# Optimization experiments

Measured on AMD Instinct MI355X. Metric: run time of the kernel, lower is better.

## Reference

```python
import jax, jax.numpy as jnp
import numpy as np

N = 50000       # original graph nodes (= number of subgraphs, one per node)
S = 10          # nodes per subgraph
M = N * S       # combined subgraph nodes
E = 2_000_000   # combined subgraph edges
E0 = 1_000_000  # original edges
NIN, HOP, NOUT, L = 64, 16, 128, 3
D = NIN + HOP   # conv width (80)


def setup_inputs() -> dict:
    key = jax.random.key(0)
    ks = iter(jax.random.split(key, 40))
    rng = np.random.default_rng(0)

    # structured index tensors: subgraph b occupies rows [b*S, (b+1)*S); row b*S is the centroid
    sub_batch = np.repeat(np.arange(N, dtype=np.int64), S)
    nodes_mapper = rng.integers(0, N, size=M, dtype=np.int64)
    nodes_mapper[::S] = np.arange(N)           # centroid: mapper == batch id
    hop_indicator = rng.integers(1, 5, size=M).astype(np.int64)
    hop_indicator[::S] = 0                     # centroid is hop 0
    edge_index = rng.integers(0, M, size=(2, E), dtype=np.int64)
    edges_mapper = rng.integers(0, E0, size=E, dtype=np.int64)

    def lin(k, fin, fout):
        return jax.random.normal(k, (fin, fout), jnp.float32) / np.sqrt(fin)

    inp = dict(
        x=jax.random.normal(next(ks), (N, NIN), jnp.float32),
        edge_attr=jax.random.normal(next(ks), (E0, D), jnp.float32),
        hop_table=jax.random.normal(next(ks), (20, HOP), jnp.float32),
        conv_W=jax.random.normal(next(ks), (L, D, D), jnp.float32) / np.sqrt(D),
        bn_g=jnp.ones((L, D), jnp.float32),
        bn_b=jnp.zeros((L, D), jnp.float32),
        oe_W0=lin(next(ks), D, NOUT), oe_b0=jnp.zeros((NOUT,), jnp.float32),
        oe_W1=lin(next(ks), NOUT, NOUT), oe_b1=jnp.zeros((NOUT,), jnp.float32),
        oe_W2=lin(next(ks), NOUT, NOUT), oe_b2=jnp.zeros((NOUT,), jnp.float32),
        st_W0=lin(next(ks), NOUT, NOUT), st_b0=jnp.zeros((NOUT,), jnp.float32),
        st_W1=lin(next(ks), NOUT, NOUT), st_b1=jnp.zeros((NOUT,), jnp.float32),
        st_W2=lin(next(ks), NOUT, NOUT), st_b2=jnp.zeros((NOUT,), jnp.float32),
        ct_W0=lin(next(ks), NOUT, NOUT), ct_b0=jnp.zeros((NOUT,), jnp.float32),
        ct_W1=lin(next(ks), NOUT, NOUT), ct_b1=jnp.zeros((NOUT,), jnp.float32),
        ct_W2=lin(next(ks), NOUT, NOUT), ct_b2=jnp.zeros((NOUT,), jnp.float32),
        gc_W=lin(next(ks), HOP, NOUT), gc_b=jnp.zeros((NOUT,), jnp.float32),
        gs_W=lin(next(ks), HOP, NOUT), gs_b=jnp.zeros((NOUT,), jnp.float32),
        gx_W=lin(next(ks), HOP, NOUT), gx_b=jnp.zeros((NOUT,), jnp.float32),
        nodes_mapper=jnp.asarray(nodes_mapper),
        edge_index=jnp.asarray(edge_index),
        edges_mapper=jnp.asarray(edges_mapper),
        sub_batch=jnp.asarray(sub_batch),
        hop_indicator=jnp.asarray(hop_indicator),
    )
    return inp


def _mlp3(h, W0, b0, W1, b1, W2, b2, final_act):
    h = jax.nn.relu(h @ W0 + b0)
    h = jax.nn.relu(h @ W1 + b1)
    h = h @ W2 + b2
    return jax.nn.relu(h) if final_act else h


def reference(x, edge_attr, hop_table, conv_W, bn_g, bn_b,
              oe_W0, oe_b0, oe_W1, oe_b1, oe_W2, oe_b2,
              st_W0, st_b0, st_W1, st_b1, st_W2, st_b2,
              ct_W0, ct_b0, ct_W1, ct_b1, ct_W2, ct_b2,
              gc_W, gc_b, gs_W, gs_b, gx_W, gx_b,
              nodes_mapper, edge_index, edges_mapper, sub_batch, hop_indicator):
    src, dst = edge_index[0], edge_index[1]
    ea = edge_attr[edges_mapper]                              # [E, D] gather
    hemb = hop_table[hop_indicator + 1]                       # [M, HOP]
    h = jnp.concatenate([x[nodes_mapper], hemb], axis=-1)     # [M, D]

    # GNN: nlayer x (GINE-style conv -> relu -> batchnorm(batch stats) -> residual)
    for l in range(L):
        msg = h[src] + ea                                     # [E, D]
        agg = jax.ops.segment_sum(msg, dst, num_segments=M)   # scatter-add
        h2 = jax.nn.relu(agg @ conv_W[l])
        mu = jnp.mean(h2, axis=0)
        var = jnp.var(h2, axis=0)
        h2 = (h2 - mu) * jax.lax.rsqrt(var + 1e-5) * bn_g[l] + bn_b[l]
        h = h2 + h                                            # residual

    # output encoder MLP (no final activation)
    h = _mlp3(h, oe_W0, oe_b0, oe_W1, oe_b1, oe_W2, oe_b2, False)  # [M, NOUT]

    # three views with sigmoid hop gates
    g_c = jax.nn.sigmoid(hemb @ gc_W + gc_b)
    g_s = jax.nn.sigmoid(hemb @ gs_W + gs_b)
    g_x = jax.nn.sigmoid(hemb @ gx_W + gx_b)

    cm = (nodes_mapper == sub_batch)[:, None]                 # centroid mask (one per subgraph)
    centroid_x = jax.ops.segment_sum(jnp.where(cm, h * g_c, 0.0), sub_batch, num_segments=N)
    subgraph_x = jax.ops.segment_sum(
        _mlp3(h, st_W0, st_b0, st_W1, st_b1, st_W2, st_b2, True) * g_s, sub_batch, num_segments=N)
    context_x = jax.ops.segment_sum(
        _mlp3(h, ct_W0, ct_b0, ct_W1, ct_b1, ct_W2, ct_b2, True) * g_x, nodes_mapper, num_segments=N)

    return centroid_x + subgraph_x + context_x                # embs_combine_mode='add'
```

## Files before the change

### kernel.cpp

```cpp
#include <hip/hip_runtime.h>


typedef __attribute__((ext_vector_type(8))) short bf16x8;
typedef __attribute__((ext_vector_type(4))) float f32x4;

static constexpr int cN = 50000;
static constexpr int cM = 500000;
static constexpr int cE = 2000000;

__device__ __forceinline__ float b2f(unsigned short u) {
  union { unsigned int u; float f; } v; v.u = ((unsigned int)u) << 16; return v.f;
}
__device__ __forceinline__ unsigned short f2b(float f) {
  union { float f; unsigned int u; } v; v.f = f;
  unsigned int x = v.u;
  x += 0x7fffu + ((x >> 16) & 1u);
  return (unsigned short)(x >> 16);
}
__device__ __forceinline__ float sigm(float x) { return 1.0f / (1.0f + __expf(-x)); }
__device__ __forceinline__ f32x4 mfma16(bf16x8 a, bf16x8 b, f32x4 c) {
  return __builtin_amdgcn_mfma_f32_16x16x32_bf16(a, b, c, 0, 0, 0);
}

struct RepackDesc { const float* src; unsigned short* dst; int K; int N; int tiles; };
struct RepackArgs { RepackDesc d[15]; };

__global__ __launch_bounds__(256) void repack_kernel(RepackArgs a) {
  RepackDesc dd = a.d[blockIdx.y];
  int tile = blockIdx.x;
  if (tile >= dd.tiles) return;
  int ncb = dd.N >> 4;
  int c = tile / ncb, cb = tile - c * ncb;
  for (int e = threadIdx.x; e < 512; e += 256) {
    int lane = e >> 3, j = e & 7;
    int k = 32 * c + 8 * (lane >> 4) + j;
    int n = 16 * cb + (lane & 15);
    unsigned short v = (k < dd.K) ? f2b(dd.src[(size_t)k * dd.N + n]) : (unsigned short)0;
    dd.dst[(size_t)tile * 512 + e] = v;
  }
}

__global__ __launch_bounds__(256) void build_h_kernel(
    const float* __restrict__ x, const float* __restrict__ ht,
    const int* __restrict__ nmap, const int* __restrict__ hop,
    unsigned short* __restrict__ h)
{
  int i = blockIdx.x * 256 + threadIdx.x;
  if (i >= cM * 20) return;
  int row = i / 20, cc = i - row * 20;
  int col = cc * 4;
  float4 f;
  if (col < 64) {
    f = *(const float4*)(x + (size_t)nmap[row] * 64 + col);
  } else {
    int hi = hop[row] + 1;
    f = *(const float4*)(ht + (size_t)hi * 16 + (col - 64));
  }
  ushort4 o; o.x = f2b(f.x); o.y = f2b(f.y); o.z = f2b(f.z); o.w = f2b(f.w);
  *(ushort4*)(h + (size_t)row * 80 + col) = o;
}

__global__ __launch_bounds__(256) void hist_kernel(const int* __restrict__ ei, int* __restrict__ deg) {
  int e = blockIdx.x * 256 + threadIdx.x;
  if (e < cE) atomicAdd(&deg[ei[cE + e]], 1);
}

__global__ __launch_bounds__(256) void scan1_kernel(const int* __restrict__ deg, int* __restrict__ bsum) {
  __shared__ int s[256];
  int i = blockIdx.x * 256 + threadIdx.x;
  s[threadIdx.x] = (i < cM) ? deg[i] : 0;
  __syncthreads();
  for (int o = 128; o > 0; o >>= 1) {
    if (threadIdx.x < o) s[threadIdx.x] += s[threadIdx.x + o];
    __syncthreads();
  }
  if (threadIdx.x == 0) bsum[blockIdx.x] = s[0];
}

__global__ void scan2_kernel(int* __restrict__ bsum, int nb) {
  if (threadIdx.x == 0 && blockIdx.x == 0) {
    int acc = 0;
    for (int i = 0; i < nb; ++i) { int t = bsum[i]; bsum[i] = acc; acc += t; }
  }
}

__global__ __launch_bounds__(256) void scan3_kernel(
    const int* __restrict__ deg, const int* __restrict__ bsum,
    int* __restrict__ rowptr, int* __restrict__ cursor)
{
  __shared__ int s[256];
  int i = blockIdx.x * 256 + threadIdx.x;
  int v = (i < cM) ? deg[i] : 0;
  s[threadIdx.x] = v;
  __syncthreads();
  for (int o = 1; o < 256; o <<= 1) {
    int t = (threadIdx.x >= o) ? s[threadIdx.x - o] : 0;
    __syncthreads();
    s[threadIdx.x] += t;
    __syncthreads();
  }
  if (i < cM) {
    int ex = bsum[blockIdx.x] + s[threadIdx.x] - v;
    rowptr[i] = ex; cursor[i] = ex;
  }
  if (i == cM - 1) rowptr[cM] = bsum[blockIdx.x] + s[threadIdx.x];
}

__global__ __launch_bounds__(256) void scatter_kernel(
    const int* __restrict__ ei, const int* __restrict__ emap,
    int* __restrict__ cursor, int* __restrict__ srcs, int* __restrict__ em2)
{
  int e = blockIdx.x * 256 + threadIdx.x;
  if (e >= cE) return;
  int d = ei[cE + e];
  int pos = atomicAdd(&cursor[d], 1);
  srcs[pos] = ei[e];
  em2[pos] = emap[e];
}

__global__ __launch_bounds__(320) void eag_rowsum_kernel(
    const float* __restrict__ ea, const int* __restrict__ em2,
    const int* __restrict__ rowptr, unsigned short* __restrict__ eag)
{
  int t = threadIdx.x;
  int r = blockIdx.x * 16 + t / 20;
  int c = (t % 20) * 4;
  if (r >= cM) return;
  int p0 = rowptr[r], p1 = rowptr[r + 1];
  float4 acc = {0.f, 0.f, 0.f, 0.f};
  for (int p = p0; p < p1; ++p) {
    int em = em2[p];
    float4 v = *(const float4*)(ea + (size_t)em * 80 + c);
    acc.x += v.x; acc.y += v.y; acc.z += v.z; acc.w += v.w;
  }
  ushort4 o = {f2b(acc.x), f2b(acc.y), f2b(acc.z), f2b(acc.w)};
  *(ushort4*)(eag + (size_t)r * 80 + c) = o;
}

__global__ __launch_bounds__(320) void aggregate_kernel(
    const unsigned short* __restrict__ h, const unsigned short* __restrict__ eag,
    const int* __restrict__ rowptr, const int* __restrict__ srcs,
    unsigned short* __restrict__ Bo)
{
  int t = threadIdx.x;
  int r = blockIdx.x * 16 + t / 20;
  int c = (t % 20) * 4;
  if (r >= cM) return;
  int p0 = rowptr[r], p1 = rowptr[r + 1];
  ushort4 a0 = *(const ushort4*)(eag + (size_t)r * 80 + c);
  float4 acc = {b2f(a0.x), b2f(a0.y), b2f(a0.z), b2f(a0.w)};
  for (int p = p0; p < p1; ++p) {
    int s = srcs[p];
    ushort4 v = *(const ushort4*)(h + (size_t)s * 80 + c);
    acc.x += b2f(v.x); acc.y += b2f(v.y); acc.z += b2f(v.z); acc.w += b2f(v.w);
  }
  ushort4 o = {f2b(acc.x), f2b(acc.y), f2b(acc.z), f2b(acc.w)};
  *(ushort4*)(Bo + (size_t)r * 80 + c) = o;
}

__global__ __launch_bounds__(256) void edge_scatter_kernel(
    const unsigned short* __restrict__ h, const float* __restrict__ ea,
    const int* __restrict__ ei, const int* __restrict__ emap,
    float* __restrict__ agg)
{
  int i = blockIdx.x * 256 + threadIdx.x;
  if (i >= cE * 20) return;
  int e = i / 20, q = i - e * 20;
  int src = ei[e], dst = ei[cE + e], em = emap[e];
  ushort4 hv = *(const ushort4*)(h + (size_t)src * 80 + q * 4);
  float4 ev = *(const float4*)(ea + (size_t)em * 80 + q * 4);
  float* ap = agg + (size_t)dst * 80 + q * 4;
  atomicAdd(ap + 0, b2f(hv.x) + ev.x);
  atomicAdd(ap + 1, b2f(hv.y) + ev.y);
  atomicAdd(ap + 2, b2f(hv.z) + ev.z);
  atomicAdd(ap + 3, b2f(hv.w) + ev.w);
}

template<bool F32IO>
__global__ __launch_bounds__(256) void conv_gemm_kernel(
    void* __restrict__ aggv, const unsigned short* __restrict__ Bp)
{
  __shared__ __align__(16) unsigned short Bl[7680];
  for (int i = threadIdx.x; i < 7680; i += 256) Bl[i] = Bp[i];
  __syncthreads();
  int lane = threadIdx.x & 63, wave = threadIdx.x >> 6;
  int tile = blockIdx.x * 4 + wave;
  bool act = tile < (cM / 16);
  int quad = lane >> 4, m = lane & 15;
  size_t rowA = (size_t)tile * 16 + m;

  bf16x8 a[3];
  #pragma unroll
  for (int c = 0; c < 3; ++c) {
    bf16x8 av = {0, 0, 0, 0, 0, 0, 0, 0};
    int k = 32 * c + 8 * quad;
    if (act && k + 8 <= 80) {
      if constexpr (F32IO) {
        const float* p = (const float*)aggv + rowA * 80 + k;
        float4 f0 = *(const float4*)p;
        float4 f1 = *(const float4*)(p + 4);
        av[0] = (short)f2b(f0.x); av[1] = (short)f2b(f0.y);
        av[2] = (short)f2b(f0.z); av[3] = (short)f2b(f0.w);
        av[4] = (short)f2b(f1.x); av[5] = (short)f2b(f1.y);
        av[6] = (short)f2b(f1.z); av[7] = (short)f2b(f1.w);
      } else {
        av = *(const bf16x8*)((const unsigned short*)aggv + rowA * 80 + k);
      }
    }
    a[c] = av;
  }

  #pragma unroll
  for (int cb = 0; cb < 5; ++cb) {
    f32x4 acc = {0.f, 0.f, 0.f, 0.f};
    #pragma unroll
    for (int c = 0; c < 3; ++c)
      acc = mfma16(a[c], *(const bf16x8*)(Bl + ((size_t)(c * 5 + cb) * 64 + lane) * 8), acc);
    int col = cb * 16 + m;
    #pragma unroll
    for (int i2 = 0; i2 < 4; ++i2) {
      size_t row = (size_t)tile * 16 + quad * 4 + i2;
      if (act) {
        float v = fmaxf(acc[i2], 0.0f);
        if constexpr (F32IO) ((float*)aggv)[row * 80 + col] = v;
        else ((unsigned short*)aggv)[row * 80 + col] = f2b(v);
      }
    }
  }
}

template<bool F32IO>
__global__ __launch_bounds__(256) void stats_kernel(
    const void* __restrict__ h2v, float* __restrict__ stats)
{
  __shared__ __align__(16) float ssum[12 * 80];
  __shared__ __align__(16) float ssq[12 * 80];
  int t = threadIdx.x;
  int cc = t % 20, slot = t / 20;
  if (slot < 12) {
    float s0 = 0, s1 = 0, s2 = 0, s3 = 0, q0 = 0, q1 = 0, q2 = 0, q3 = 0;
    for (int row = blockIdx.x * 12 + slot; row < cM; row += gridDim.x * 12) {
      float f0, f1, f2, f3;
      if constexpr (F32IO) {
        float4 v = *(const float4*)((const float*)h2v + (size_t)row * 80 + cc * 4);
        f0 = v.x; f1 = v.y; f2 = v.z; f3 = v.w;
      } else {
        ushort4 v = *(const ushort4*)((const unsigned short*)h2v + (size_t)row * 80 + cc * 4);
        f0 = b2f(v.x); f1 = b2f(v.y); f2 = b2f(v.z); f3 = b2f(v.w);
      }
      s0 += f0; s1 += f1; s2 += f2; s3 += f3;
      q0 += f0 * f0; q1 += f1 * f1; q2 += f2 * f2; q3 += f3 * f3;
    }
    int base = slot * 80 + cc * 4;
    ssum[base + 0] = s0; ssum[base + 1] = s1; ssum[base + 2] = s2; ssum[base + 3] = s3;
    ssq[base + 0] = q0; ssq[base + 1] = q1; ssq[base + 2] = q2; ssq[base + 3] = q3;
  }
  __syncthreads();
  if (t < 20) {
    for (int j = 0; j < 4; ++j) {
      int c = t * 4 + j;
      float s = 0, q = 0;
      for (int sl = 0; sl < 12; ++sl) { s += ssum[sl * 80 + c]; q += ssq[sl * 80 + c]; }
      atomicAdd(&stats[c], s);
      atomicAdd(&stats[80 + c], q);
    }
  }
}

template<bool F32IO>
__global__ __launch_bounds__(256) void bn_residual_kernel(
    const void* __restrict__ h2v, const float* __restrict__ stats,
    const float* __restrict__ g, const float* __restrict__ b,
    unsigned short* __restrict__ h)
{
  int i = blockIdx.x * 256 + threadIdx.x;
  if (i >= cM * 20) return;
  int row = i / 20, cc = i - row * 20;
  int col = cc * 4;
  float in2[4];
  if constexpr (F32IO) {
    float4 v2 = *(const float4*)((const float*)h2v + (size_t)row * 80 + col);
    in2[0] = v2.x; in2[1] = v2.y; in2[2] = v2.z; in2[3] = v2.w;
  } else {
    ushort4 v2 = *(const ushort4*)((const unsigned short*)h2v + (size_t)row * 80 + col);
    in2[0] = b2f(v2.x); in2[1] = b2f(v2.y); in2[2] = b2f(v2.z); in2[3] = b2f(v2.w);
  }
  ushort4 vh = *(const ushort4*)(h + (size_t)row * 80 + col);
  const float invM = 1.0f / (float)cM;
  unsigned short inh[4] = {vh.x, vh.y, vh.z, vh.w};
  unsigned short o[4];
  #pragma unroll
  for (int j = 0; j < 4; ++j) {
    int c = col + j;
    float mu = stats[c] * invM;
    float var = fmaxf(stats[80 + c] * invM - mu * mu, 0.0f);
    float inv = rsqrtf(var + 1e-5f);
    float val = (in2[j] - mu) * inv * g[c] + b[c] + b2f(inh[j]);
    o[j] = f2b(val);
  }
  ushort4 ov = {o[0], o[1], o[2], o[3]};
  *(ushort4*)(h + (size_t)row * 80 + col) = ov;
}

template<int KCH>
__device__ __forceinline__ void layer_to_tb(
    const bf16x8* a, const unsigned short* Wl, const float* biasl,
    unsigned short* tbw, int lane)
{
  int quad = lane >> 4, m = lane & 15;
  #pragma unroll
  for (int cb = 0; cb < 8; ++cb) {
    f32x4 acc = {0.f, 0.f, 0.f, 0.f};
    #pragma unroll
    for (int c = 0; c < KCH; ++c)
      acc = mfma16(a[c], *(const bf16x8*)(Wl + ((size_t)(c * 8 + cb) * 64 + lane) * 8), acc);
    int col = cb * 16 + m;
    float bv = biasl[col];
    #pragma unroll
    for (int i2 = 0; i2 < 4; ++i2)
      tbw[(quad * 4 + i2) * 136 + col] = f2b(fmaxf(acc[i2] + bv, 0.0f));
  }
}

__device__ __forceinline__ void tb_to_a(bf16x8* a, const unsigned short* tbw, int lane) {
  int quad = lane >> 4, m = lane & 15;
  #pragma unroll
  for (int c = 0; c < 4; ++c)
    a[c] = *(const bf16x8*)(tbw + m * 136 + 32 * c + 8 * quad);
}

__device__ __forceinline__ bf16x8 load_hemb(const float* ht, int hi, int quad) {
  bf16x8 he = {0, 0, 0, 0, 0, 0, 0, 0};
  if (quad < 2) {
    const float* p = ht + (size_t)hi * 16 + 8 * quad;
    float4 f0 = *(const float4*)p;
    float4 f1 = *(const float4*)(p + 4);
    he[0] = (short)f2b(f0.x); he[1] = (short)f2b(f0.y);
    he[2] = (short)f2b(f0.z); he[3] = (short)f2b(f0.w);
    he[4] = (short)f2b(f1.x); he[5] = (short)f2b(f1.y);
    he[6] = (short)f2b(f1.z); he[7] = (short)f2b(f1.w);
  }
  return he;
}

__global__ __launch_bounds__(256) void oe_fused_kernel(
    const unsigned short* __restrict__ h,
    const unsigned short* __restrict__ P0, const float* __restrict__ b0,
    const unsigned short* __restrict__ P1, const float* __restrict__ b1,
    const unsigned short* __restrict__ P2, const float* __restrict__ b2,
    unsigned short* __restrict__ Out)
{
  __shared__ __align__(16) unsigned short Wbuf[16384];
  __shared__ __align__(16) float bias[3][128];
  __shared__ __align__(16) unsigned short tb[4][16 * 136];
  int t = threadIdx.x;
  for (int i = t; i < 12288; i += 256) Wbuf[i] = P0[i];
  if (t < 128) { bias[0][t] = b0[t]; bias[1][t] = b1[t]; bias[2][t] = b2[t]; }
  __syncthreads();

  int lane = t & 63, wave = t >> 6;
  int tile = blockIdx.x * 4 + wave;
  bool act = tile < (cM / 16);
  int quad = lane >> 4, m = lane & 15;
  size_t rowA = (size_t)tile * 16 + m;

  bf16x8 a[4];
  #pragma unroll
  for (int c = 0; c < 4; ++c) {
    bf16x8 av = {0, 0, 0, 0, 0, 0, 0, 0};
    int k = 32 * c + 8 * quad;
    if (act && c < 3 && k + 8 <= 80)
      av = *(const bf16x8*)(h + rowA * 80 + k);
    a[c] = av;
  }
  layer_to_tb<3>(a, Wbuf, bias[0], tb[wave], lane);
  __syncthreads();
  tb_to_a(a, tb[wave], lane);
  for (int i = t; i < 16384; i += 256) Wbuf[i] = P1[i];
  __syncthreads();
  layer_to_tb<4>(a, Wbuf, bias[1], tb[wave], lane);
  __syncthreads();
  tb_to_a(a, tb[wave], lane);
  for (int i = t; i < 16384; i += 256) Wbuf[i] = P2[i];
  __syncthreads();

  #pragma unroll
  for (int cb = 0; cb < 8; ++cb) {
    f32x4 acc = {0.f, 0.f, 0.f, 0.f};
    #pragma unroll
    for (int c = 0; c < 4; ++c)
      acc = mfma16(a[c], *(const bf16x8*)(Wbuf + ((size_t)(c * 8 + cb) * 64 + lane) * 8), acc);
    int col = cb * 16 + m;
    float bv = bias[2][col];
    #pragma unroll
    for (int i2 = 0; i2 < 4; ++i2) {
      size_t row = (size_t)tile * 16 + quad * 4 + i2;
      if (act) Out[row * 128 + col] = f2b(acc[i2] + bv);
    }
  }
}

__global__ __launch_bounds__(256) void st_fused_kernel(
    const unsigned short* __restrict__ hout,
    const unsigned short* __restrict__ P0, const float* __restrict__ b0,
    const unsigned short* __restrict__ P1, const float* __restrict__ b1,
    const unsigned short* __restrict__ P2, const float* __restrict__ b2,
    const unsigned short* __restrict__ Gs, const float* __restrict__ gsb,
    const unsigned short* __restrict__ Gc, const float* __restrict__ gcb,
    const float* __restrict__ ht, const int* __restrict__ hop,
    const int* __restrict__ nmap, const int* __restrict__ sb,
    float* __restrict__ outp)
{
  __shared__ __align__(16) unsigned short Wbuf[16384];
  __shared__ __align__(16) float bias[5][128];
  __shared__ __align__(16) unsigned short tb[4][16 * 136];
  int t = threadIdx.x;
  for (int i = t; i < 16384; i += 256) Wbuf[i] = P0[i];
  if (t < 128) {
    bias[0][t] = b0[t]; bias[1][t] = b1[t]; bias[2][t] = b2[t];
    bias[3][t] = gsb[t]; bias[4][t] = gcb[t];
  }
  __syncthreads();

  int lane = t & 63, wave = t >> 6;
  int tile = blockIdx.x * 4 + wave;
  bool act = tile < (cM / 16);
  int quad = lane >> 4, m = lane & 15;
  size_t rowA = (size_t)tile * 16 + m;

  bf16x8 a[4];
  #pragma unroll
  for (int c = 0; c < 4; ++c) {
    bf16x8 av = {0, 0, 0, 0, 0, 0, 0, 0};
    if (act) av = *(const bf16x8*)(hout + rowA * 128 + 32 * c + 8 * quad);
    a[c] = av;
  }
  layer_to_tb<4>(a, Wbuf, bias[0], tb[wave], lane);
  __syncthreads();
  tb_to_a(a, tb[wave], lane);
  for (int i = t; i < 16384; i += 256) Wbuf[i] = P1[i];
  __syncthreads();
  layer_to_tb<4>(a, Wbuf, bias[1], tb[wave], lane);
  __syncthreads();
  tb_to_a(a, tb[wave], lane);
  for (int i = t; i < 16384; i += 256) Wbuf[i] = P2[i];
  __syncthreads();
  float* red = (float*)&tb[0][0];
  for (int i = t; i < 1024; i += 256) red[i] = 0.0f;
  int sbBase = sb[blockIdx.x * 64];
  __syncthreads();

  int hi = act ? (hop[rowA] + 1) : 0;
  bf16x8 he = load_hemb(ht, hi, quad);

  int r[4], sbr[4]; bool mk[4];
  #pragma unroll
  for (int i2 = 0; i2 < 4; ++i2) {
    int row = tile * 16 + quad * 4 + i2;
    r[i2] = row;
    sbr[i2] = act ? sb[row] : 0;
    mk[i2] = act && (nmap[row] == sbr[i2]);
  }

  #pragma unroll
  for (int cb = 0; cb < 8; ++cb) {
    f32x4 acc = {0.f, 0.f, 0.f, 0.f}, ga = {0.f, 0.f, 0.f, 0.f}, ca = {0.f, 0.f, 0.f, 0.f};
    #pragma unroll
    for (int c = 0; c < 4; ++c)
      acc = mfma16(a[c], *(const bf16x8*)(Wbuf + ((size_t)(c * 8 + cb) * 64 + lane) * 8), acc);
    ga = mfma16(he, *(const bf16x8*)(Gs + ((size_t)cb * 64 + lane) * 8), ga);
    ca = mfma16(he, *(const bf16x8*)(Gc + ((size_t)cb * 64 + lane) * 8), ca);
    int col = cb * 16 + m;
    #pragma unroll
    for (int i2 = 0; i2 < 4; ++i2) {
      float v = fmaxf(acc[i2] + bias[2][col], 0.0f) * sigm(ga[i2] + bias[3][col]);
      if (mk[i2]) v += b2f(hout[(size_t)r[i2] * 128 + col]) * sigm(ca[i2] + bias[4][col]);
      if (act) {
        int slot = sbr[i2] - sbBase;
        if ((unsigned)slot < 8u) atomicAdd(&red[slot * 128 + col], v);
        else atomicAdd(outp + (size_t)sbr[i2] * 128 + col, v);
      }
    }
  }

  __syncthreads();
  for (int i = t; i < 1024; i += 256) {
    float v = red[i];
    if (v != 0.0f)
      atomicAdd(outp + (size_t)(sbBase + (i >> 7)) * 128 + (i & 127), v);
  }
}

__global__ __launch_bounds__(256) void ct_fused_kernel(
    const unsigned short* __restrict__ hout,
    const unsigned short* __restrict__ P0, const float* __restrict__ b0,
    const unsigned short* __restrict__ P1, const float* __restrict__ b1,
    const unsigned short* __restrict__ P2, const float* __restrict__ b2,
    const unsigned short* __restrict__ Gx, const float* __restrict__ gxb,
    const float* __restrict__ ht, const int* __restrict__ hop,
    const int* __restrict__ nmap,
    float* __restrict__ outp)
{
  __shared__ __align__(16) unsigned short Wbuf[16384];
  __shared__ __align__(16) float bias[4][128];
  __shared__ __align__(16) unsigned short tb[4][16 * 136];
  int t = threadIdx.x;
  for (int i = t; i < 16384; i += 256) Wbuf[i] = P0[i];
  if (t < 128) {
    bias[0][t] = b0[t]; bias[1][t] = b1[t];
    bias[2][t] = b2[t]; bias[3][t] = gxb[t];
  }
  __syncthreads();

  int lane = t & 63, wave = t >> 6;
  int tile = blockIdx.x * 4 + wave;
  bool act = tile < (cM / 16);
  int quad = lane >> 4, m = lane & 15;
  size_t rowA = (size_t)tile * 16 + m;

  bf16x8 a[4];
  #pragma unroll
  for (int c = 0; c < 4; ++c) {
    bf16x8 av = {0, 0, 0, 0, 0, 0, 0, 0};
    if (act) av = *(const bf16x8*)(hout + rowA * 128 + 32 * c + 8 * quad);
    a[c] = av;
  }
  layer_to_tb<4>(a, Wbuf, bias[0], tb[wave], lane);
  __syncthreads();
  tb_to_a(a, tb[wave], lane);
  for (int i = t; i < 16384; i += 256) Wbuf[i] = P1[i];
  __syncthreads();
  layer_to_tb<4>(a, Wbuf, bias[1], tb[wave], lane);
  __syncthreads();
  tb_to_a(a, tb[wave], lane);
  for (int i = t; i < 16384; i += 256) Wbuf[i] = P2[i];
  __syncthreads();

  int hi = act ? (hop[rowA] + 1) : 0;
  bf16x8 he = load_hemb(ht, hi, quad);

  int dst[4];
  #pragma unroll
  for (int i2 = 0; i2 < 4; ++i2) {
    int row = tile * 16 + quad * 4 + i2;
    dst[i2] = act ? nmap[row] : 0;
  }

  #pragma unroll
  for (int cb = 0; cb < 8; ++cb) {
    f32x4 acc = {0.f, 0.f, 0.f, 0.f}, ga = {0.f, 0.f, 0.f, 0.f};
    #pragma unroll
    for (int c = 0; c < 4; ++c)
      acc = mfma16(a[c], *(const bf16x8*)(Wbuf + ((size_t)(c * 8 + cb) * 64 + lane) * 8), acc);
    ga = mfma16(he, *(const bf16x8*)(Gx + ((size_t)cb * 64 + lane) * 8), ga);
    int col = cb * 16 + m;
    #pragma unroll
    for (int i2 = 0; i2 < 4; ++i2) {
      float v = fmaxf(acc[i2] + bias[2][col], 0.0f) * sigm(ga[i2] + bias[3][col]);
      if (act) atomicAdd(outp + (size_t)dst[i2] * 128 + col, v);
    }
  }
}

extern "C" void kernel_launch(void* const* d_in, const int* in_sizes, int n_in,
                              void* d_out, int out_size, void* d_ws, size_t ws_size,
                              hipStream_t stream)
{
  const float* x     = (const float*)d_in[0];
  const float* eattr = (const float*)d_in[1];
  const float* htab  = (const float*)d_in[2];
  const float* convW = (const float*)d_in[3];
  const float* bng   = (const float*)d_in[4];
  const float* bnb   = (const float*)d_in[5];
  const float* oeW0 = (const float*)d_in[6];  const float* oeb0 = (const float*)d_in[7];
  const float* oeW1 = (const float*)d_in[8];  const float* oeb1 = (const float*)d_in[9];
  const float* oeW2 = (const float*)d_in[10]; const float* oeb2 = (const float*)d_in[11];
  const float* stW0 = (const float*)d_in[12]; const float* stb0 = (const float*)d_in[13];
  const float* stW1 = (const float*)d_in[14]; const float* stb1 = (const float*)d_in[15];
  const float* stW2 = (const float*)d_in[16]; const float* stb2 = (const float*)d_in[17];
  const float* ctW0 = (const float*)d_in[18]; const float* ctb0 = (const float*)d_in[19];
  const float* ctW1 = (const float*)d_in[20]; const float* ctb1 = (const float*)d_in[21];
  const float* ctW2 = (const float*)d_in[22]; const float* ctb2 = (const float*)d_in[23];
  const float* gcW = (const float*)d_in[24]; const float* gcb = (const float*)d_in[25];
  const float* gsW = (const float*)d_in[26]; const float* gsb = (const float*)d_in[27];
  const float* gxW = (const float*)d_in[28]; const float* gxb = (const float*)d_in[29];
  const int* nmap = (const int*)d_in[30];
  const int* ei   = (const int*)d_in[31];
  const int* emap = (const int*)d_in[32];
  const int* sb   = (const int*)d_in[33];
  const int* hop  = (const int*)d_in[34];

  if (n_in < 35 ||
      in_sizes[0] != cN * 64 || in_sizes[1] != 1000000 * 80 ||
      in_sizes[2] != 20 * 16 || in_sizes[3] != 3 * 80 * 80 ||
      in_sizes[30] != cM || in_sizes[31] != 2 * cE || in_sizes[32] != cE ||
      in_sizes[33] != cM || in_sizes[34] != cM || out_size != cN * 128)
    return;

  const size_t PCONV0 = 0, PCONV1 = 7680, PCONV2 = 15360, POE0 = 23040,
               POE1 = 35328, POE2 = 51712, PST0 = 68096, PST1 = 84480,
               PST2 = 100864, PCT0 = 117248, PCT1 = 133632, PCT2 = 150016,
               PGC = 166400, PGS = 170496, PGX = 174592;
  const size_t PACK_BYTES = 178688 * 2 + 256;

  char* ws = (char*)d_ws;
  size_t off = 0;
  auto alloc = [&](size_t bytes) -> void* {
    void* p = ws + off; off += (bytes + 255) & ~(size_t)255; return p;
  };

  unsigned short* h    = (unsigned short*)alloc((size_t)cM * 80 * 2);
  unsigned short* Aeag = (unsigned short*)alloc((size_t)cM * 80 * 2);
  unsigned short* Bagg = (unsigned short*)alloc((size_t)cM * 80 * 2);
  int*   rowptr = (int*)alloc((size_t)(cM + 1) * 4);
  int*   srcs   = (int*)alloc((size_t)cE * 4);
  float* stats  = (float*)alloc(1024);
  unsigned short* packs = (unsigned short*)alloc(PACK_BYTES);
  size_t needFast = off;
  bool fast = (ws_size >= needFast);

  float* aggF = nullptr;
  if (!fast) {
    off = 0;
    h     = (unsigned short*)alloc((size_t)cM * 80 * 2);
    aggF  = (float*)alloc((size_t)cM * 80 * 4);
    stats = (float*)alloc(1024);
    packs = (unsigned short*)alloc(PACK_BYTES);
    if (ws_size < off) return;
  }

  RepackArgs ra;
  auto setd = [&](int idx, const float* src, size_t dstOff, int K, int Nn, int tiles) {
    ra.d[idx].src = src; ra.d[idx].dst = packs + dstOff;
    ra.d[idx].K = K; ra.d[idx].N = Nn; ra.d[idx].tiles = tiles;
  };
  setd(0, convW,          PCONV0, 80, 80, 15);
  setd(1, convW + 6400,   PCONV1, 80, 80, 15);
  setd(2, convW + 12800,  PCONV2, 80, 80, 15);
  setd(3, oeW0, POE0, 80, 128, 24);
  setd(4, oeW1, POE1, 128, 128, 32);
  setd(5, oeW2, POE2, 128, 128, 32);
  setd(6, stW0, PST0, 128, 128, 32);
  setd(7, stW1, PST1, 128, 128, 32);
  setd(8, stW2, PST2, 128, 128, 32);
  setd(9, ctW0, PCT0, 128, 128, 32);
  setd(10, ctW1, PCT1, 128, 128, 32);
  setd(11, ctW2, PCT2, 128, 128, 32);
  setd(12, gcW, PGC, 16, 128, 8);
  setd(13, gsW, PGS, 16, 128, 8);
  setd(14, gxW, PGX, 16, 128, 8);
  repack_kernel<<<dim3(32, 15), 256, 0, stream>>>(ra);

  const int elemBlocksM = (cM * 20 + 255) / 256;
  const int gemmBlocks  = (cM / 16 + 3) / 4;
  const int rowBlocks   = (cM + 15) / 16;
  const int edgeB256    = (cE + 255) / 256;
  const int scanBlocks  = (cM + 255) / 256;

  build_h_kernel<<<elemBlocksM, 256, 0, stream>>>(x, htab, nmap, hop, h);
  hipMemsetAsync(d_out, 0, (size_t)cN * 128 * 4, stream);

  unsigned short* hout;

  if (fast) {
    int* deg    = (int*)Bagg;
    int* cursor = deg + cM;
    int* em2    = cursor + cM;
    int* bsum   = em2 + cE;

    hipMemsetAsync(deg, 0, (size_t)cM * 4, stream);
    hist_kernel<<<edgeB256, 256, 0, stream>>>(ei, deg);
    scan1_kernel<<<scanBlocks, 256, 0, stream>>>(deg, bsum);
    scan2_kernel<<<1, 64, 0, stream>>>(bsum, scanBlocks);
    scan3_kernel<<<scanBlocks, 256, 0, stream>>>(deg, bsum, rowptr, cursor);
    scatter_kernel<<<edgeB256, 256, 0, stream>>>(ei, emap, cursor, srcs, em2);
    eag_rowsum_kernel<<<rowBlocks, 320, 0, stream>>>(eattr, em2, rowptr, Aeag);

    for (int l = 0; l < 3; ++l) {
      aggregate_kernel<<<rowBlocks, 320, 0, stream>>>(h, Aeag, rowptr, srcs, Bagg);
      conv_gemm_kernel<false><<<gemmBlocks, 256, 0, stream>>>(
          Bagg, packs + (l == 0 ? PCONV0 : l == 1 ? PCONV1 : PCONV2));
      hipMemsetAsync(stats, 0, 160 * 4, stream);
      stats_kernel<false><<<1024, 256, 0, stream>>>(Bagg, stats);
      bn_residual_kernel<false><<<elemBlocksM, 256, 0, stream>>>(
          Bagg, stats, bng + l * 80, bnb + l * 80, h);
    }
    hout = Aeag;
  } else {
    const int edgeBlocks = (cE * 20) / 256;
    for (int l = 0; l < 3; ++l) {
      hipMemsetAsync(aggF, 0, (size_t)cM * 80 * 4, stream);
      edge_scatter_kernel<<<edgeBlocks, 256, 0, stream>>>(h, eattr, ei, emap, aggF);
      conv_gemm_kernel<true><<<gemmBlocks, 256, 0, stream>>>(
          aggF, packs + (l == 0 ? PCONV0 : l == 1 ? PCONV1 : PCONV2));
      hipMemsetAsync(stats, 0, 160 * 4, stream);
      stats_kernel<true><<<1024, 256, 0, stream>>>(aggF, stats);
      bn_residual_kernel<true><<<elemBlocksM, 256, 0, stream>>>(
          aggF, stats, bng + l * 80, bnb + l * 80, h);
    }
    hout = (unsigned short*)aggF;
  }

  oe_fused_kernel<<<gemmBlocks, 256, 0, stream>>>(
      h, packs + POE0, oeb0, packs + POE1, oeb1, packs + POE2, oeb2, hout);

  st_fused_kernel<<<gemmBlocks, 256, 0, stream>>>(
      hout, packs + PST0, stb0, packs + PST1, stb1, packs + PST2, stb2,
      packs + PGS, gsb, packs + PGC, gcb, htab, hop, nmap, sb, (float*)d_out);

  ct_fused_kernel<<<gemmBlocks, 256, 0, stream>>>(
      hout, packs + PCT0, ctb0, packs + PCT1, ctb1, packs + PCT2, ctb2,
      packs + PGX, gxb, htab, hop, nmap, (float*)d_out);
}
```

Measured before the change: 2.920 ms.

## Process four row tiles per wave to amortize weight staging in MLP kernels

```diff
diff --git a/kernel.cpp b/kernel.cpp
--- a/kernel.cpp
+++ b/kernel.cpp
@@ -7,6 +7,7 @@
 static constexpr int cN = 50000;
 static constexpr int cM = 500000;
 static constexpr int cE = 2000000;
+static constexpr int cTiles = cM / 16;
 
 __device__ __forceinline__ float b2f(unsigned short u) {
   union { unsigned int u; float f; } v; v.u = ((unsigned int)u) << 16; return v.f;
@@ -181,49 +182,60 @@
     void* __restrict__ aggv, const unsigned short* __restrict__ Bp)
 {
   __shared__ __align__(16) unsigned short Bl[7680];
-  for (int i = threadIdx.x; i < 7680; i += 256) Bl[i] = Bp[i];
+  #pragma unroll
+  for (int i = threadIdx.x; i < 960; i += 256)
+    ((uint4*)Bl)[i] = ((const uint4*)Bp)[i];
   __syncthreads();
   int lane = threadIdx.x & 63, wave = threadIdx.x >> 6;
-  int tile = blockIdx.x * 4 + wave;
-  bool act = tile < (cM / 16);
+  int tile0 = (blockIdx.x * 4 + wave) * 4;
   int quad = lane >> 4, m = lane & 15;
-  size_t rowA = (size_t)tile * 16 + m;
-
-  bf16x8 a[3];
-  #pragma unroll
-  for (int c = 0; c < 3; ++c) {
-    bf16x8 av = {0, 0, 0, 0, 0, 0, 0, 0};
-    int k = 32 * c + 8 * quad;
-    if (act && k + 8 <= 80) {
-      if constexpr (F32IO) {
-        const float* p = (const float*)aggv + rowA * 80 + k;
-        float4 f0 = *(const float4*)p;
-        float4 f1 = *(const float4*)(p + 4);
-        av[0] = (short)f2b(f0.x); av[1] = (short)f2b(f0.y);
-        av[2] = (short)f2b(f0.z); av[3] = (short)f2b(f0.w);
-        av[4] = (short)f2b(f1.x); av[5] = (short)f2b(f1.y);
-        av[6] = (short)f2b(f1.z); av[7] = (short)f2b(f1.w);
-      } else {
-        av = *(const bf16x8*)((const unsigned short*)aggv + rowA * 80 + k);
+
+  bf16x8 a[4][3];
+  #pragma unroll
+  for (int tt = 0; tt < 4; ++tt) {
+    int tile = tile0 + tt;
+    bool act = tile < cTiles;
+    size_t rowA = (size_t)tile * 16 + m;
+    #pragma unroll
+    for (int c = 0; c < 3; ++c) {
+      bf16x8 av = {0, 0, 0, 0, 0, 0, 0, 0};
+      int k = 32 * c + 8 * quad;
+      if (act && k + 8 <= 80) {
+        if constexpr (F32IO) {
+          const float* p = (const float*)aggv + rowA * 80 + k;
+          float4 f0 = *(const float4*)p;
+          float4 f1 = *(const float4*)(p + 4);
+          av[0] = (short)f2b(f0.x); av[1] = (short)f2b(f0.y);
+          av[2] = (short)f2b(f0.z); av[3] = (short)f2b(f0.w);
+          av[4] = (short)f2b(f1.x); av[5] = (short)f2b(f1.y);
+          av[6] = (short)f2b(f1.z); av[7] = (short)f2b(f1.w);
+        } else {
+          av = *(const bf16x8*)((const unsigned short*)aggv + rowA * 80 + k);
+        }
       }
-    }
-    a[c] = av;
-  }
-
-  #pragma unroll
-  for (int cb = 0; cb < 5; ++cb) {
-    f32x4 acc = {0.f, 0.f, 0.f, 0.f};
-    #pragma unroll
-    for (int c = 0; c < 3; ++c)
-      acc = mfma16(a[c], *(const bf16x8*)(Bl + ((size_t)(c * 5 + cb) * 64 + lane) * 8), acc);
-    int col = cb * 16 + m;
-    #pragma unroll
-    for (int i2 = 0; i2 < 4; ++i2) {
-      size_t row = (size_t)tile * 16 + quad * 4 + i2;
-      if (act) {
-        float v = fmaxf(acc[i2], 0.0f);
-        if constexpr (F32IO) ((float*)aggv)[row * 80 + col] = v;
-        else ((unsigned short*)aggv)[row * 80 + col] = f2b(v);
+      a[tt][c] = av;
+    }
+  }
+
+  #pragma unroll
+  for (int tt = 0; tt < 4; ++tt) {
+    int tile = tile0 + tt;
+    bool act = tile < cTiles;
+    #pragma unroll
+    for (int cb = 0; cb < 5; ++cb) {
+      f32x4 acc = {0.f, 0.f, 0.f, 0.f};
+      #pragma unroll
+      for (int c = 0; c < 3; ++c)
+        acc = mfma16(a[tt][c], *(const bf16x8*)(Bl + ((size_t)(c * 5 + cb) * 64 + lane) * 8), acc);
+      int col = cb * 16 + m;
+      #pragma unroll
+      for (int i2 = 0; i2 < 4; ++i2) {
+        size_t row = (size_t)tile * 16 + quad * 4 + i2;
+        if (act) {
+          float v = fmaxf(acc[i2], 0.0f);
+          if constexpr (F32IO) ((float*)aggv)[row * 80 + col] = v;
+          else ((unsigned short*)aggv)[row * 80 + col] = f2b(v);
+        }
       }
     }
   }
@@ -354,48 +366,67 @@
   __shared__ __align__(16) float bias[3][128];
   __shared__ __align__(16) unsigned short tb[4][16 * 136];
   int t = threadIdx.x;
-  for (int i = t; i < 12288; i += 256) Wbuf[i] = P0[i];
+  #pragma unroll
+  for (int i = t; i < 1536; i += 256) ((uint4*)Wbuf)[i] = ((const uint4*)P0)[i];
   if (t < 128) { bias[0][t] = b0[t]; bias[1][t] = b1[t]; bias[2][t] = b2[t]; }
   __syncthreads();
 
   int lane = t & 63, wave = t >> 6;
-  int tile = blockIdx.x * 4 + wave;
-  bool act = tile < (cM / 16);
+  int tile0 = (blockIdx.x * 4 + wave) * 4;
   int quad = lane >> 4, m = lane & 15;
-  size_t rowA = (size_t)tile * 16 + m;
-
-  bf16x8 a[4];
-  #pragma unroll
-  for (int c = 0; c < 4; ++c) {
-    bf16x8 av = {0, 0, 0, 0, 0, 0, 0, 0};
-    int k = 32 * c + 8 * quad;
-    if (act && c < 3 && k + 8 <= 80)
-      av = *(const bf16x8*)(h + rowA * 80 + k);
-    a[c] = av;
-  }
-  layer_to_tb<3>(a, Wbuf, bias[0], tb[wave], lane);
-  __syncthreads();
-  tb_to_a(a, tb[wave], lane);
-  for (int i = t; i < 16384; i += 256) Wbuf[i] = P1[i];
-  __syncthreads();
-  layer_to_tb<4>(a, Wbuf, bias[1], tb[wave], lane);
-  __syncthreads();
-  tb_to_a(a, tb[wave], lane);
-  for (int i = t; i < 16384; i += 256) Wbuf[i] = P2[i];
-  __syncthreads();
-
-  #pragma unroll
-  for (int cb = 0; cb < 8; ++cb) {
-    f32x4 acc = {0.f, 0.f, 0.f, 0.f};
-    #pragma unroll
-    for (int c = 0; c < 4; ++c)
-      acc = mfma16(a[c], *(const bf16x8*)(Wbuf + ((size_t)(c * 8 + cb) * 64 + lane) * 8), acc);
-    int col = cb * 16 + m;
-    float bv = bias[2][col];
-    #pragma unroll
-    for (int i2 = 0; i2 < 4; ++i2) {
-      size_t row = (size_t)tile * 16 + quad * 4 + i2;
-      if (act) Out[row * 128 + col] = f2b(acc[i2] + bv);
+
+  bf16x8 a[4][4];
+  #pragma unroll
+  for (int tt = 0; tt < 4; ++tt) {
+    int tile = tile0 + tt;
+    bool act = tile < cTiles;
+    size_t rowA = (size_t)tile * 16 + m;
+    #pragma unroll
+    for (int c = 0; c < 4; ++c) {
+      bf16x8 av = {0, 0, 0, 0, 0, 0, 0, 0};
+      int k = 32 * c + 8 * quad;
+      if (act && c < 3 && k + 8 <= 80)
+        av = *(const bf16x8*)(h + rowA * 80 + k);
+      a[tt][c] = av;
+    }
+  }
+
+  #pragma unroll
+  for (int tt = 0; tt < 4; ++tt) {
+    layer_to_tb<3>(a[tt], Wbuf, bias[0], tb[wave], lane);
+    tb_to_a(a[tt], tb[wave], lane);
+  }
+  __syncthreads();
+  #pragma unroll
+  for (int i = t; i < 2048; i += 256) ((uint4*)Wbuf)[i] = ((const uint4*)P1)[i];
+  __syncthreads();
+  #pragma unroll
+  for (int tt = 0; tt < 4; ++tt) {
+    layer_to_tb<4>(a[tt], Wbuf, bias[1], tb[wave], lane);
+    tb_to_a(a[tt], tb[wave], lane);
+  }
+  __syncthreads();
+  #pragma unroll
+  for (int i = t; i < 2048; i += 256) ((uint4*)Wbuf)[i] = ((const uint4*)P2)[i];
+  __syncthreads();
+
+  #pragma unroll
+  for (int tt = 0; tt < 4; ++tt) {
+    int tile = tile0 + tt;
+    bool act = tile < cTiles;
+    #pragma unroll
+    for (int cb = 0; cb < 8; ++cb) {
+      f32x4 acc = {0.f, 0.f, 0.f, 0.f};
+      #pragma unroll
+      for (int c = 0; c < 4; ++c)
+        acc = mfma16(a[tt][c], *(const bf16x8*)(Wbuf + ((size_t)(c * 8 + cb) * 64 + lane) * 8), acc);
+      int col = cb * 16 + m;
+      float bv = bias[2][col];
+      #pragma unroll
+      for (int i2 = 0; i2 < 4; ++i2) {
+        size_t row = (size_t)tile * 16 + quad * 4 + i2;
+        if (act) Out[row * 128 + col] = f2b(acc[i2] + bv);
+      }
     }
   }
 }
@@ -415,7 +446,8 @@
   __shared__ __align__(16) float bias[5][128];
   __shared__ __align__(16) unsigned short tb[4][16 * 136];
   int t = threadIdx.x;
-  for (int i = t; i < 16384; i += 256) Wbuf[i] = P0[i];
+  #pragma unroll
+  for (int i = t; i < 2048; i += 256) ((uint4*)Wbuf)[i] = ((const uint4*)P0)[i];
   if (t < 128) {
     bias[0][t] = b0[t]; bias[1][t] = b1[t]; bias[2][t] = b2[t];
     bias[3][t] = gsb[t]; bias[4][t] = gcb[t];
@@ -423,68 +455,86 @@
   __syncthreads();
 
   int lane = t & 63, wave = t >> 6;
-  int tile = blockIdx.x * 4 + wave;
-  bool act = tile < (cM / 16);
+  int tile0 = (blockIdx.x * 4 + wave) * 4;
   int quad = lane >> 4, m = lane & 15;
-  size_t rowA = (size_t)tile * 16 + m;
-
-  bf16x8 a[4];
-  #pragma unroll
-  for (int c = 0; c < 4; ++c) {
-    bf16x8 av = {0, 0, 0, 0, 0, 0, 0, 0};
-    if (act) av = *(const bf16x8*)(hout + rowA * 128 + 32 * c + 8 * quad);
-    a[c] = av;
-  }
-  layer_to_tb<4>(a, Wbuf, bias[0], tb[wave], lane);
-  __syncthreads();
-  tb_to_a(a, tb[wave], lane);
-  for (int i = t; i < 16384; i += 256) Wbuf[i] = P1[i];
-  __syncthreads();
-  layer_to_tb<4>(a, Wbuf, bias[1], tb[wave], lane);
-  __syncthreads();
-  tb_to_a(a, tb[wave], lane);
-  for (int i = t; i < 16384; i += 256) Wbuf[i] = P2[i];
-  __syncthreads();
+
+  bf16x8 a[4][4];
+  #pragma unroll
+  for (int tt = 0; tt < 4; ++tt) {
+    int tile = tile0 + tt;
+    bool act = tile < cTiles;
+    size_t rowA = (size_t)tile * 16 + m;
+    #pragma unroll
+    for (int c = 0; c < 4; ++c) {
+      bf16x8 av = {0, 0, 0, 0, 0, 0, 0, 0};
+      if (act) av = *(const bf16x8*)(hout + rowA * 128 + 32 * c + 8 * quad);
+      a[tt][c] = av;
+    }
+  }
+
+  #pragma unroll
+  for (int tt = 0; tt < 4; ++tt) {
+    layer_to_tb<4>(a[tt], Wbuf, bias[0], tb[wave], lane);
+    tb_to_a(a[tt], tb[wave], lane);
+  }
+  __syncthreads();
+  #pragma unroll
+  for (int i = t; i < 2048; i += 256) ((uint4*)Wbuf)[i] = ((const uint4*)P1)[i];
+  __syncthreads();
+  #pragma unroll
+  for (int tt = 0; tt < 4; ++tt) {
+    layer_to_tb<4>(a[tt], Wbuf, bias[1], tb[wave], lane);
+    tb_to_a(a[tt], tb[wave], lane);
+  }
+  __syncthreads();
+  #pragma unroll
+  for (int i = t; i < 2048; i += 256) ((uint4*)Wbuf)[i] = ((const uint4*)P2)[i];
   float* red = (float*)&tb[0][0];
-  for (int i = t; i < 1024; i += 256) red[i] = 0.0f;
-  int sbBase = sb[blockIdx.x * 64];
-  __syncthreads();
-
-  int hi = act ? (hop[rowA] + 1) : 0;
-  bf16x8 he = load_hemb(ht, hi, quad);
-
-  int r[4], sbr[4]; bool mk[4];
-  #pragma unroll
-  for (int i2 = 0; i2 < 4; ++i2) {
-    int row = tile * 16 + quad * 4 + i2;
-    r[i2] = row;
-    sbr[i2] = act ? sb[row] : 0;
-    mk[i2] = act && (nmap[row] == sbr[i2]);
-  }
-
-  #pragma unroll
-  for (int cb = 0; cb < 8; ++cb) {
-    f32x4 acc = {0.f, 0.f, 0.f, 0.f}, ga = {0.f, 0.f, 0.f, 0.f}, ca = {0.f, 0.f, 0.f, 0.f};
-    #pragma unroll
-    for (int c = 0; c < 4; ++c)
-      acc = mfma16(a[c], *(const bf16x8*)(Wbuf + ((size_t)(c * 8 + cb) * 64 + lane) * 8), acc);
-    ga = mfma16(he, *(const bf16x8*)(Gs + ((size_t)cb * 64 + lane) * 8), ga);
-    ca = mfma16(he, *(const bf16x8*)(Gc + ((size_t)cb * 64 + lane) * 8), ca);
-    int col = cb * 16 + m;
+  for (int i = t; i < 4096; i += 256) red[i] = 0.0f;
+  int sbBase = sb[blockIdx.x * 256];
+  __syncthreads();
+
+  #pragma unroll
+  for (int tt = 0; tt < 4; ++tt) {
+    int tile = tile0 + tt;
+    bool act = tile < cTiles;
+    size_t rowA = (size_t)tile * 16 + m;
+    int hi = act ? (hop[rowA] + 1) : 0;
+    bf16x8 he = load_hemb(ht, hi, quad);
+
+    int r[4], sbr[4]; bool mk[4];
     #pragma unroll
     for (int i2 = 0; i2 < 4; ++i2) {
-      float v = fmaxf(acc[i2] + bias[2][col], 0.0f) * sigm(ga[i2] + bias[3][col]);
-      if (mk[i2]) v += b2f(hout[(size_t)r[i2] * 128 + col]) * sigm(ca[i2] + bias[4][col]);
-      if (act) {
-        int slot = sbr[i2] - sbBase;
-        if ((unsigned)slot < 8u) atomicAdd(&red[slot * 128 + col], v);
-        else atomicAdd(outp + (size_t)sbr[i2] * 128 + col, v);
+      int row = tile * 16 + quad * 4 + i2;
+      r[i2] = row;
+      sbr[i2] = act ? sb[row] : 0;
+      mk[i2] = act && (nmap[row] == sbr[i2]);
+    }
+
+    #pragma unroll
+    for (int cb = 0; cb < 8; ++cb) {
+      f32x4 acc = {0.f, 0.f, 0.f, 0.f}, ga = {0.f, 0.f, 0.f, 0.f}, ca = {0.f, 0.f, 0.f, 0.f};
+      #pragma unroll
+      for (int c = 0; c < 4; ++c)
+        acc = mfma16(a[tt][c], *(const bf16x8*)(Wbuf + ((size_t)(c * 8 + cb) * 64 + lane) * 8), acc);
+      ga = mfma16(he, *(const bf16x8*)(Gs + ((size_t)cb * 64 + lane) * 8), ga);
+      ca = mfma16(he, *(const bf16x8*)(Gc + ((size_t)cb * 64 + lane) * 8), ca);
+      int col = cb * 16 + m;
+      #pragma unroll
+      for (int i2 = 0; i2 < 4; ++i2) {
+        float v = fmaxf(acc[i2] + bias[2][col], 0.0f) * sigm(ga[i2] + bias[3][col]);
+        if (mk[i2]) v += b2f(hout[(size_t)r[i2] * 128 + col]) * sigm(ca[i2] + bias[4][col]);
+        if (act) {
+          int slot = sbr[i2] - sbBase;
+          if ((unsigned)slot < 32u) atomicAdd(&red[slot * 128 + col], v);
+          else atomicAdd(outp + (size_t)sbr[i2] * 128 + col, v);
+        }
       }
     }
   }
 
   __syncthreads();
-  for (int i = t; i < 1024; i += 256) {
+  for (int i = t; i < 4096; i += 256) {
     float v = red[i];
     if (v != 0.0f)
       atomicAdd(outp + (size_t)(sbBase + (i >> 7)) * 128 + (i & 127), v);
@@ -505,7 +555,8 @@
   __shared__ __align__(16) float bias[4][128];
   __shared__ __align__(16) unsigned short tb[4][16 * 136];
   int t = threadIdx.x;
-  for (int i = t; i < 16384; i += 256) Wbuf[i] = P0[i];
+  #pragma unroll
+  for (int i = t; i < 2048; i += 256) ((uint4*)Wbuf)[i] = ((const uint4*)P0)[i];
   if (t < 128) {
     bias[0][t] = b0[t]; bias[1][t] = b1[t];
     bias[2][t] = b2[t]; bias[3][t] = gxb[t];
@@ -513,51 +564,70 @@
   __syncthreads();
 
   int lane = t & 63, wave = t >> 6;
-  int tile = blockIdx.x * 4 + wave;
-  bool act = tile < (cM / 16);
+  int tile0 = (blockIdx.x * 4 + wave) * 4;
   int quad = lane >> 4, m = lane & 15;
-  size_t rowA = (size_t)tile * 16 + m;
-
-  bf16x8 a[4];
-  #pragma unroll
-  for (int c = 0; c < 4; ++c) {
-    bf16x8 av = {0, 0, 0, 0, 0, 0, 0, 0};
-    if (act) av = *(const bf16x8*)(hout + rowA * 128 + 32 * c + 8 * quad);
-    a[c] = av;
-  }
-  layer_to_tb<4>(a, Wbuf, bias[0], tb[wave], lane);
-  __syncthreads();
-  tb_to_a(a, tb[wave], lane);
-  for (int i = t; i < 16384; i += 256) Wbuf[i] = P1[i];
-  __syncthreads();
-  layer_to_tb<4>(a, Wbuf, bias[1], tb[wave], lane);
-  __syncthreads();
-  tb_to_a(a, tb[wave], lane);
-  for (int i = t; i < 16384; i += 256) Wbuf[i] = P2[i];
-  __syncthreads();
-
-  int hi = act ? (hop[rowA] + 1) : 0;
-  bf16x8 he = load_hemb(ht, hi, quad);
-
-  int dst[4];
-  #pragma unroll
-  for (int i2 = 0; i2 < 4; ++i2) {
-    int row = tile * 16 + quad * 4 + i2;
-    dst[i2] = act ? nmap[row] : 0;
-  }
-
-  #pragma unroll
-  for (int cb = 0; cb < 8; ++cb) {
-    f32x4 acc = {0.f, 0.f, 0.f, 0.f}, ga = {0.f, 0.f, 0.f, 0.f};
-    #pragma unroll
-    for (int c = 0; c < 4; ++c)
-      acc = mfma16(a[c], *(const bf16x8*)(Wbuf + ((size_t)(c * 8 + cb) * 64 + lane) * 8), acc);
-    ga = mfma16(he, *(const bf16x8*)(Gx + ((size_t)cb * 64 + lane) * 8), ga);
-    int col = cb * 16 + m;
+
+  bf16x8 a[4][4];
+  #pragma unroll
+  for (int tt = 0; tt < 4; ++tt) {
+    int tile = tile0 + tt;
+    bool act = tile < cTiles;
+    size_t rowA = (size_t)tile * 16 + m;
+    #pragma unroll
+    for (int c = 0; c < 4; ++c) {
+      bf16x8 av = {0, 0, 0, 0, 0, 0, 0, 0};
+      if (act) av = *(const bf16x8*)(hout + rowA * 128 + 32 * c + 8 * quad);
+      a[tt][c] = av;
+    }
+  }
+
+  #pragma unroll
+  for (int tt = 0; tt < 4; ++tt) {
+    layer_to_tb<4>(a[tt], Wbuf, bias[0], tb[wave], lane);
+    tb_to_a(a[tt], tb[wave], lane);
+  }
+  __syncthreads();
+  #pragma unroll
+  for (int i = t; i < 2048; i += 256) ((uint4*)Wbuf)[i] = ((const uint4*)P1)[i];
+  __syncthreads();
+  #pragma unroll
+  for (int tt = 0; tt < 4; ++tt) {
+    layer_to_tb<4>(a[tt], Wbuf, bias[1], tb[wave], lane);
+    tb_to_a(a[tt], tb[wave], lane);
+  }
+  __syncthreads();
+  #pragma unroll
+  for (int i = t; i < 2048; i += 256) ((uint4*)Wbuf)[i] = ((const uint4*)P2)[i];
+  __syncthreads();
+
+  #pragma unroll
+  for (int tt = 0; tt < 4; ++tt) {
+    int tile = tile0 + tt;
+    bool act = tile < cTiles;
+    size_t rowA = (size_t)tile * 16 + m;
+    int hi = act ? (hop[rowA] + 1) : 0;
+    bf16x8 he = load_hemb(ht, hi, quad);
+
+    int dst[4];
     #pragma unroll
     for (int i2 = 0; i2 < 4; ++i2) {
-      float v = fmaxf(acc[i2] + bias[2][col], 0.0f) * sigm(ga[i2] + bias[3][col]);
-      if (act) atomicAdd(outp + (size_t)dst[i2] * 128 + col, v);
+      int row = tile * 16 + quad * 4 + i2;
+      dst[i2] = act ? nmap[row] : 0;
+    }
+
+    #pragma unroll
+    for (int cb = 0; cb < 8; ++cb) {
+      f32x4 acc = {0.f, 0.f, 0.f, 0.f}, ga = {0.f, 0.f, 0.f, 0.f};
+      #pragma unroll
+      for (int c = 0; c < 4; ++c)
+        acc = mfma16(a[tt][c], *(const bf16x8*)(Wbuf + ((size_t)(c * 8 + cb) * 64 + lane) * 8), acc);
+      ga = mfma16(he, *(const bf16x8*)(Gx + ((size_t)cb * 64 + lane) * 8), ga);
+      int col = cb * 16 + m;
+      #pragma unroll
+      for (int i2 = 0; i2 < 4; ++i2) {
+        float v = fmaxf(acc[i2] + bias[2][col], 0.0f) * sigm(ga[i2] + bias[3][col]);
+        if (act) atomicAdd(outp + (size_t)dst[i2] * 128 + col, v);
+      }
     }
   }
 }
@@ -652,7 +722,7 @@
   repack_kernel<<<dim3(32, 15), 256, 0, stream>>>(ra);
 
   const int elemBlocksM = (cM * 20 + 255) / 256;
-  const int gemmBlocks  = (cM / 16 + 3) / 4;
+  const int mlpBlocks   = (cTiles + 15) / 16;
   const int rowBlocks   = (cM + 15) / 16;
   const int edgeB256    = (cE + 255) / 256;
   const int scanBlocks  = (cM + 255) / 256;
@@ -678,7 +748,7 @@
 
     for (int l = 0; l < 3; ++l) {
       aggregate_kernel<<<rowBlocks, 320, 0, stream>>>(h, Aeag, rowptr, srcs, Bagg);
-      conv_gemm_kernel<false><<<gemmBlocks, 256, 0, stream>>>(
+      conv_gemm_kernel<false><<<mlpBlocks, 256, 0, stream>>>(
           Bagg, packs + (l == 0 ? PCONV0 : l == 1 ? PCONV1 : PCONV2));
       hipMemsetAsync(stats, 0, 160 * 4, stream);
       stats_kernel<false><<<1024, 256, 0, stream>>>(Bagg, stats);
@@ -691,7 +761,7 @@
     for (int l = 0; l < 3; ++l) {
       hipMemsetAsync(aggF, 0, (size_t)cM * 80 * 4, stream);
       edge_scatter_kernel<<<edgeBlocks, 256, 0, stream>>>(h, eattr, ei, emap, aggF);
-      conv_gemm_kernel<true><<<gemmBlocks, 256, 0, stream>>>(
+      conv_gemm_kernel<true><<<mlpBlocks, 256, 0, stream>>>(
           aggF, packs + (l == 0 ? PCONV0 : l == 1 ? PCONV1 : PCONV2));
       hipMemsetAsync(stats, 0, 160 * 4, stream);
       stats_kernel<true><<<1024, 256, 0, stream>>>(aggF, stats);
@@ -701,14 +771,14 @@
     hout = (unsigned short*)aggF;
   }
 
-  oe_fused_kernel<<<gemmBlocks, 256, 0, stream>>>(
+  oe_fused_kernel<<<mlpBlocks, 256, 0, stream>>>(
       h, packs + POE0, oeb0, packs + POE1, oeb1, packs + POE2, oeb2, hout);
 
-  st_fused_kernel<<<gemmBlocks, 256, 0, stream>>>(
+  st_fused_kernel<<<mlpBlocks, 256, 0, stream>>>(
       hout, packs + PST0, stb0, packs + PST1, stb1, packs + PST2, stb2,
       packs + PGS, gsb, packs + PGC, gcb, htab, hop, nmap, sb, (float*)d_out);
 
-  ct_fused_kernel<<<gemmBlocks, 256, 0, stream>>>(
+  ct_fused_kernel<<<mlpBlocks, 256, 0, stream>>>(
       hout, packs + PCT0, ctb0, packs + PCT1, ctb1, packs + PCT2, ctb2,
       packs + PGX, gxb, htab, hop, nmap, (float*)d_out);
 }
```

Measured after the change: 2.936 ms. Within noise of the previous version (+0.5%).
